# Performance work log

Hardware: AMD Instinct MI355X
Metric: run time of the kernel (lower is better)

## Reference

```python
import jax, jax.numpy as jnp
import numpy as np

B, T, C, K = 1024, 500, 64, 2000  # batch, timesteps, latent chains (KCs), observed KCs
S, O = 2, 2                       # n_states, n_outputs (hard-coded in BktModel)


def setup_inputs() -> dict:
    key = jax.random.key(0)
    k1, k2, k3, k4, k5, k6 = jax.random.split(key, 6)
    corr = jax.random.randint(k1, (B, T), 0, O)
    kc = jax.random.randint(k2, (B, T), 0, K)
    # soft KC-membership matrix (stands in for gumbel_softmax sample; rows sum to 1)
    A = jax.nn.softmax(jax.random.normal(k3, (K, C)), axis=1)
    trans_logits = jax.random.normal(k4, (C, S, S))
    obs_logits = jax.random.normal(k5, (C, S, O))
    init_logits = jax.random.normal(k6, (C, S))
    return dict(corr=corr, kc=kc, A=A, trans_logits=trans_logits,
                obs_logits=obs_logits, init_logits=init_logits)


def _hmm_forward(obs, chain, trans_logits, obs_logits, init_logits):
    # obs: [B,T] int, chain: [B,T,C] float
    n_batch = obs.shape[0]
    log_obs = jax.nn.log_softmax(obs_logits, axis=2)   # [C,S,O]
    log_t = jax.nn.log_softmax(trans_logits, axis=1)   # [C,S,S] (normalized over dim 1, as in torch)
    log_alpha0 = jnp.tile(jax.nn.log_softmax(init_logits, axis=1)[None], (n_batch, 1, 1))  # [B,C,S]

    def step(log_alpha, xs):
        y, cc = xs  # y: [B] int, cc: [B,C]
        # predictive distribution over outputs
        a1 = jnp.einsum('bc,cso->bso', cc, log_obs)          # [B,S,O]
        a2 = jnp.einsum('bc,bcs->bs', cc, log_alpha)         # [B,S]
        log_py = jax.scipy.special.logsumexp(a1 + a2[:, :, None], axis=1)  # [B,O]
        log_py = jax.nn.log_softmax(log_py, axis=1)
        # state update for the active chains
        lo_y = jnp.transpose(log_obs[:, :, y], (2, 0, 1))    # [B,C,S]
        lp = jnp.einsum('bcs,bc->bs', lo_y, cc)              # [B,S]
        a1c = jnp.einsum('bcs,bc->bs', log_alpha, cc)        # [B,S]
        a2c = jnp.einsum('bc,cst->bst', cc, log_t)           # [B,S,S]
        a3 = jax.scipy.special.logsumexp(lp[:, None, :] + a1c[:, None, :] + a2c, axis=2)  # [B,S]
        new_la = (1.0 - cc)[:, :, None] * log_alpha + cc[:, :, None] * a3[:, None, :]
        return new_la, log_py

    _, outs = jax.lax.scan(step, log_alpha0,
                           (obs.T, jnp.transpose(chain, (1, 0, 2))))
    return jnp.transpose(outs, (1, 0, 2))  # [B,T,O]


def reference(corr, kc, A, trans_logits, obs_logits, init_logits):
    chain = A[kc]  # [B,T,C]
    return _hmm_forward(corr, chain, trans_logits, obs_logits, init_logits)
```

## Files before the change

kernel.cpp:

```cpp
#include <hip/hip_runtime.h>
#include <math.h>

#define BB 1024
#define TT 500
#define CC_ 64
#define KK 2000

#define LOG2E 1.44269504088896340736f
#define LN2   0.69314718055994530942f

typedef float f32x4 __attribute__((ext_vector_type(4)));
typedef float f32x2 __attribute__((ext_vector_type(2)));

#if __has_builtin(__builtin_amdgcn_exp2f)
__device__ __forceinline__ float fast_exp2(float x) { return __builtin_amdgcn_exp2f(x); }
#else
__device__ __forceinline__ float fast_exp2(float x) { return exp2f(x); }
#endif
#if __has_builtin(__builtin_amdgcn_logf)
__device__ __forceinline__ float fast_log2(float x) { return __builtin_amdgcn_logf(x); }
#else
__device__ __forceinline__ float fast_log2(float x) { return log2f(x); }
#endif

__device__ __forceinline__ float lse2_2(float a, float b) {
    float m = fmaxf(a, b);
    float d = fminf(a, b) - m;
    return m + fast_log2(1.0f + fast_exp2(d));
}

template<int CTRL, int RM, int BM>
__device__ __forceinline__ float dpp_add(float x) {
    int s = __builtin_amdgcn_update_dpp(0, __float_as_int(x), CTRL, RM, BM, true);
    return x + __int_as_float(s);
}
__device__ __forceinline__ float wave_sum63(float x) {
    x = dpp_add<0x111, 0xf, 0xf>(x);
    x = dpp_add<0x112, 0xf, 0xf>(x);
    x = dpp_add<0x114, 0xf, 0xf>(x);
    x = dpp_add<0x118, 0xf, 0xf>(x);
    x = dpp_add<0x142, 0xa, 0xf>(x);
    x = dpp_add<0x143, 0xc, 0xf>(x);
    return x;
}
__device__ __forceinline__ float rowsum16(float x) {
    x = dpp_add<0x121, 0xf, 0xf>(x);
    x = dpp_add<0x122, 0xf, 0xf>(x);
    x = dpp_add<0x124, 0xf, 0xf>(x);
    x = dpp_add<0x128, 0xf, 0xf>(x);
    return x;
}

__global__ __launch_bounds__(64) void precompute_P(
    const float* __restrict__ A,
    const float* __restrict__ trans_logits,
    const float* __restrict__ obs_logits,
    float* __restrict__ PA,
    float* __restrict__ P3)
{
    int k = blockIdx.x;
    int c = threadIdx.x;

    float ob[2][2];
#pragma unroll
    for (int s = 0; s < 2; ++s) {
        float o0 = obs_logits[c * 4 + s * 2 + 0] * LOG2E;
        float o1 = obs_logits[c * 4 + s * 2 + 1] * LOG2E;
        float l = lse2_2(o0, o1);
        ob[s][0] = o0 - l;
        ob[s][1] = o1 - l;
    }
    float lt[2][2];
    {
        float t00 = trans_logits[c * 4 + 0] * LOG2E;
        float t01 = trans_logits[c * 4 + 1] * LOG2E;
        float t10 = trans_logits[c * 4 + 2] * LOG2E;
        float t11 = trans_logits[c * 4 + 3] * LOG2E;
        float l0 = lse2_2(t00, t10);
        float l1 = lse2_2(t01, t11);
        lt[0][0] = t00 - l0; lt[0][1] = t01 - l1;
        lt[1][0] = t10 - l0; lt[1][1] = t11 - l1;
    }

    float a = A[k * CC_ + c];
    float v[8];
    v[0] = a * ob[0][0]; v[1] = a * ob[0][1];
    v[2] = a * ob[1][0]; v[3] = a * ob[1][1];
    v[4] = a * lt[0][0]; v[5] = a * lt[0][1];
    v[6] = a * lt[1][0]; v[7] = a * lt[1][1];

#pragma unroll
    for (int i = 0; i < 8; ++i) v[i] = wave_sum63(v[i]);
    if (c == 63) {
        ((float4*)PA)[k] = make_float4(v[0], v[1], v[2], v[3]);
#pragma unroll
        for (int y = 0; y < 2; ++y) {
            float sel0 = v[y];
            float sel1 = v[2 + y];
            ((float4*)P3)[k * 2 + y] = make_float4(
                fast_exp2(sel0 + v[4]),
                fast_exp2(sel0 + v[6]),
                sel1 + v[5],
                sel1 + v[7]);
        }
    }
}

__global__ __launch_bounds__(64, 1) void bkt_main(
    const int* __restrict__ corr,
    const int* __restrict__ kc,
    const float* __restrict__ A,
    const float* __restrict__ init_logits,
    const float* __restrict__ P3,
    float* __restrict__ out)
{
    int lane = threadIdx.x;
    int g = lane >> 4, i = lane & 15;
    int b = blockIdx.x * 4 + g;
    int bTT  = b * TT;
    int bTT4 = bTT * 4;
    int bTT8 = bTT * 8;
    int i16  = i * 16;

    f32x2 la2[4];
#pragma unroll
    for (int j = 0; j < 4; ++j) {
        float i0 = init_logits[(4 * i + j) * 2 + 0] * LOG2E;
        float i1 = init_logits[(4 * i + j) * 2 + 1] * LOG2E;
        float l = lse2_2(i0, i1);
        la2[j].x = i0 - l;
        la2[j].y = i1 - l;
    }

    int   kq[8], yq[8];
    f32x4 ccq[8], pq[8];

#pragma unroll
    for (int q = 0; q < 8; ++q) {
        asm volatile("global_load_dword %0, %2, %3\n\t"
                     "global_load_dword %1, %2, %4"
                     : "=&v"(kq[q]), "=&v"(yq[q])
                     : "v"(bTT4 + q * 4), "s"(kc), "s"(corr));
    }
#pragma unroll
    for (int q = 0; q < 8; ++q)
        asm volatile("s_waitcnt vmcnt(0)" : "+v"(kq[q]), "+v"(yq[q]));
#pragma unroll
    for (int q = 0; q < 6; ++q) {
        int va = (kq[q] << 8) + i16;
        int vp = ((kq[q] << 1) + yq[q]) << 4;
        asm volatile("global_load_dwordx4 %0, %1, %2" : "=&v"(ccq[q]) : "v"(va), "s"(A));
        asm volatile("global_load_dwordx4 %0, %1, %2" : "=&v"(pq[q])  : "v"(vp), "s"(P3));
    }
#pragma unroll
    for (int q = 0; q < 5; ++q) {
        asm volatile("global_load_dword %0, %2, %3\n\t"
                     "global_load_dword %1, %2, %4"
                     : "=&v"(kq[q]), "=&v"(yq[q])
                     : "v"(bTT4 + (8 + q) * 4), "s"(kc), "s"(corr));
    }
#pragma unroll
    for (int q = 0; q < 5; ++q)
        asm volatile("s_waitcnt vmcnt(0)" : "+v"(kq[q]), "+v"(yq[q]));
#pragma unroll
    for (int q = 0; q < 6; ++q)
        asm volatile("s_waitcnt vmcnt(0)" : "+v"(ccq[q]), "+v"(pq[q]));

    for (int tt = 0; tt <= 496; tt += 8) {
#pragma unroll
        for (int j = 0; j < 8; ++j) {
            int t = tt + j;
            int t13 = t + 13; if (t13 > TT - 1) t13 = TT - 1;
            asm volatile("global_load_dword %0, %2, %3\n\t"
                         "global_load_dword %1, %2, %4"
                         : "=&v"(kq[(j + 5) & 7]), "=&v"(yq[(j + 5) & 7])
                         : "v"(bTT4 + t13 * 4), "s"(kc), "s"(corr));
            int k6 = kq[(j + 6) & 7], y6 = yq[(j + 6) & 7];
            int va = (k6 << 8) + i16;
            int vp = ((k6 << 1) + y6) << 4;
            asm volatile("global_load_dwordx4 %0, %1, %2"
                         : "=&v"(ccq[(j + 6) & 7]) : "v"(va), "s"(A));
            asm volatile("global_load_dwordx4 %0, %1, %2"
                         : "=&v"(pq[(j + 6) & 7]) : "v"(vp), "s"(P3));
            asm volatile("s_waitcnt vmcnt(30)"
                         : "+v"(ccq[j]), "+v"(pq[j]),
                           "+v"(kq[(j + 7) & 7]), "+v"(yq[(j + 7) & 7]));

            f32x4 cc = ccq[j];
            f32x4 pr = pq[j];

            f32x2 x01 = la2[0] * cc.x + la2[1] * cc.y
                      + la2[2] * cc.z + la2[3] * cc.w;
            float x0 = rowsum16(x01.x);
            float x1 = rowsum16(x01.y);

            float d   = x1 - x0;
            float a30 = fast_log2(pr.x + fast_exp2(pr.z + d));
            float a31 = fast_log2(pr.y + fast_exp2(pr.w + d));
            f32x2 a3; a3.x = a30; a3.y = a31;

            {
                f32x2 gg;
                gg = la2[0] - x0; la2[0] = gg + (a3 - gg) * cc.x;
                gg = la2[1] - x0; la2[1] = gg + (a3 - gg) * cc.y;
                gg = la2[2] - x0; la2[2] = gg + (a3 - gg) * cc.z;
                gg = la2[3] - x0; la2[3] = gg + (a3 - gg) * cc.w;
            }

            if (t < TT) {
                f32x2 o; o.x = x0; o.y = x1;
                asm volatile("global_store_dwordx2 %1, %0, %2"
                             :: "v"(o), "v"(bTT8 + t * 8), "s"(out));
            }
        }
    }
}

__global__ __launch_bounds__(256) void finish_py(
    const int* __restrict__ kc,
    const float* __restrict__ PA,
    float* __restrict__ out)
{
    int idx = blockIdx.x * 256 + threadIdx.x;
    if (idx >= BB * TT) return;
    int k = kc[idx];
    float2 r  = ((const float2*)out)[idx];
    float4 pa = ((const float4*)PA)[k];
    float lo0 = lse2_2(pa.x + r.x, pa.z + r.y);
    float lo1 = lse2_2(pa.y + r.x, pa.w + r.y);
    float lz  = lse2_2(lo0, lo1);
    ((float2*)out)[idx] = make_float2((lo0 - lz) * LN2, (lo1 - lz) * LN2);
}

extern "C" void kernel_launch(void* const* d_in, const int* in_sizes, int n_in,
                              void* d_out, int out_size, void* d_ws, size_t ws_size,
                              hipStream_t stream) {
    const int* corr    = (const int*)d_in[0];
    const int* kc      = (const int*)d_in[1];
    const float* A     = (const float*)d_in[2];
    const float* trans = (const float*)d_in[3];
    const float* obs   = (const float*)d_in[4];
    const float* init  = (const float*)d_in[5];
    float* out = (float*)d_out;

    float* PA = (float*)d_ws;
    float* P3 = PA + KK * 4;

    precompute_P<<<KK, 64, 0, stream>>>(A, trans, obs, PA, P3);
    bkt_main<<<BB / 4, 64, 0, stream>>>(corr, kc, A, init, P3, out);
    finish_py<<<(BB * TT + 255) / 256, 256, 0, stream>>>(kc, PA, out);
}
```

Measured before the change: 83.92 us.

## Precompute next-step chain projection to take the reduction off the serial critical path

The projection x01 for step t+1 is now computed algebraically from the current log_alpha and the next step's chain weights (cc1 - cc1*cc and cc*cc1 terms), before the state update. The cross-lane rowsum reductions then no longer depend on the freshly updated log_alpha, which breaks the reduction→logsumexp→update dependency chain within each timestep. In exchange it adds two extra rowsum reductions per step and waits one step earlier on the prefetched A rows (vmcnt lowered from 30 to 24). It also changes floating-point summation order.

```diff
diff --git a/kernel.cpp b/kernel.cpp
--- a/kernel.cpp
+++ b/kernel.cpp
@@ -166,6 +166,14 @@
     for (int q = 0; q < 6; ++q)
         asm volatile("s_waitcnt vmcnt(0)" : "+v"(ccq[q]), "+v"(pq[q]));
 
+    f32x2 x01;
+    {
+        f32x4 c0 = ccq[0];
+        f32x2 s = la2[0] * c0.x + la2[1] * c0.y + la2[2] * c0.z + la2[3] * c0.w;
+        x01.x = rowsum16(s.x);
+        x01.y = rowsum16(s.y);
+    }
+
     for (int tt = 0; tt <= 496; tt += 8) {
 #pragma unroll
         for (int j = 0; j < 8; ++j) {
@@ -182,36 +190,45 @@
                          : "=&v"(ccq[(j + 6) & 7]) : "v"(va), "s"(A));
             asm volatile("global_load_dwordx4 %0, %1, %2"
                          : "=&v"(pq[(j + 6) & 7]) : "v"(vp), "s"(P3));
-            asm volatile("s_waitcnt vmcnt(30)"
-                         : "+v"(ccq[j]), "+v"(pq[j]),
+            asm volatile("s_waitcnt vmcnt(24)"
+                         : "+v"(ccq[j]), "+v"(pq[j]), "+v"(ccq[(j + 1) & 7]),
                            "+v"(kq[(j + 7) & 7]), "+v"(yq[(j + 7) & 7]));
 
-            f32x4 cc = ccq[j];
-            f32x4 pr = pq[j];
-
-            f32x2 x01 = la2[0] * cc.x + la2[1] * cc.y
-                      + la2[2] * cc.z + la2[3] * cc.w;
-            float x0 = rowsum16(x01.x);
-            float x1 = rowsum16(x01.y);
-
-            float d   = x1 - x0;
+            f32x4 cc  = ccq[j];
+            f32x4 pr  = pq[j];
+            f32x4 cc1 = ccq[(j + 1) & 7];
+
+            f32x4 uv = cc1 - cc1 * cc;
+            f32x4 mv = cc * cc1;
+            f32x2 t1 = la2[0] * uv.x + la2[1] * uv.y
+                     + la2[2] * uv.z + la2[3] * uv.w;
+            float T1x = rowsum16(t1.x);
+            float T1y = rowsum16(t1.y);
+            float S2  = rowsum16((uv.x + uv.y) + (uv.z + uv.w));
+            float S3  = rowsum16((mv.x + mv.y) + (mv.z + mv.w));
+
+            float d   = x01.y - x01.x;
             float a30 = fast_log2(pr.x + fast_exp2(pr.z + d));
             float a31 = fast_log2(pr.y + fast_exp2(pr.w + d));
-            f32x2 a3; a3.x = a30; a3.y = a31;
-
-            {
-                f32x2 gg;
-                gg = la2[0] - x0; la2[0] = gg + (a3 - gg) * cc.x;
-                gg = la2[1] - x0; la2[1] = gg + (a3 - gg) * cc.y;
-                gg = la2[2] - x0; la2[2] = gg + (a3 - gg) * cc.z;
-                gg = la2[3] - x0; la2[3] = gg + (a3 - gg) * cc.w;
+            f32x2 a3n; a3n.x = a30; a3n.y = a31;
+            float x0t = x01.x;
+
+            if (t < TT) {
+                asm volatile("global_store_dwordx2 %1, %0, %2"
+                             :: "v"(x01), "v"(bTT8 + t * 8), "s"(out));
             }
 
-            if (t < TT) {
-                f32x2 o; o.x = x0; o.y = x1;
-                asm volatile("global_store_dwordx2 %1, %0, %2"
-                             :: "v"(o), "v"(bTT8 + t * 8), "s"(out));
-            }
+            f32x2 T1v; T1v.x = T1x; T1v.y = T1y;
+            f32x2 x01n = T1v - x0t * S2;
+            x01n = x01n + a3n * S3;
+
+            f32x2 gg;
+            gg = la2[0] - x0t; la2[0] = gg + (a3n - gg) * cc.x;
+            gg = la2[1] - x0t; la2[1] = gg + (a3n - gg) * cc.y;
+            gg = la2[2] - x0t; la2[2] = gg + (a3n - gg) * cc.z;
+            gg = la2[3] - x0t; la2[3] = gg + (a3n - gg) * cc.w;
+
+            x01 = x01n;
         }
     }
 }
```

New measurement: 103.2 us. +23.0%, slower.
